# Kernel tuning notes

Measured on AMD Instinct MI355X. Metric: run time of the kernel, lower is better.

Reference implementation:

```python
import jax, jax.numpy as jnp
import numpy as np

IN_F, OUT_F, K, BATCH = 1024, 1024, 8, 4096


def setup_inputs() -> dict:
    key = jax.random.key(0)
    kx, ka, kb = jax.random.split(key, 3)
    x = jax.random.normal(kx, (BATCH, IN_F), dtype=jnp.float32)
    scale = 1.0 / (K * OUT_F)
    # a/b params: uniform in (-1,1)/(K*out_features), laid out [out, in, K]
    a = (2.0 * jax.random.uniform(ka, (OUT_F, IN_F, K)) - 1.0) * scale
    b = (2.0 * jax.random.uniform(kb, (OUT_F, IN_F, K)) - 1.0) * scale
    return {"x": x, "a": a.astype(jnp.float32), "b": b.astype(jnp.float32)}


def reference(x, a, b):
    # Fourier basis: k = 0..K-1 applied to every input feature
    K_ = a.shape[-1]
    ks = jnp.arange(K_, dtype=x.dtype)  # [K]
    phase = x[..., None] * ks  # [B, in, K]
    x_sin = jnp.sin(phase)
    x_cos = jnp.cos(phase)
    # y[b,o] = sum_{i,k} sin(k x_bi) a_oik + cos(k x_bi) b_oik
    y = jnp.einsum("bik,oik->bo", x_sin, a) + jnp.einsum("bik,oik->bo", x_cos, b)
    return y
```

## Files before the change

### kernel.cpp

```cpp
#include <hip/hip_runtime.h>

#define BATCH   4096
#define IN_F    1024
#define OUT_F   1024
#define KF      8
#define KD      14336

#define BM 256
#define BN 256
#define BK 64
#define KSPLIT 4
#define KCHUNK (KD/KSPLIT)
#define NT (KCHUNK/BK)
#define C_ELEMS ((size_t)BATCH * OUT_F)

#define QW 1040384.0f
#define DQ (1.0f/132128768.0f)

typedef int   i32x4 __attribute__((ext_vector_type(4)));
typedef float f32x4 __attribute__((ext_vector_type(4)));

__device__ __forceinline__ void gload_lds16(const void* g, void* l) {
  __builtin_amdgcn_global_load_lds((const __attribute__((address_space(1))) void*)g,
                                   (__attribute__((address_space(3))) void*)l,
                                   16, 0, 0);
}

__device__ __forceinline__ unsigned int pack4(int q0, int q1, int q2, int q3) {
  return (unsigned int)(q0 & 255) | ((unsigned int)(q1 & 255) << 8) |
         ((unsigned int)(q2 & 255) << 16) | ((unsigned int)(q3 & 255) << 24);
}

__global__ __launch_bounds__(256) void wconv_kernel(const float* __restrict__ a,
                                                    const float* __restrict__ b,
                                                    signed char* __restrict__ W,
                                                    float* __restrict__ bias) {
  const int o  = blockIdx.x;
  const int i0 = threadIdx.x * 4;
  const float4* ap = reinterpret_cast<const float4*>(a + (size_t)o * 8192 + i0 * 8);
  const float4* bp = reinterpret_cast<const float4*>(b + (size_t)o * 8192 + i0 * 8);
  union { float4 v[2]; float f[8]; } ua[4], ub[4];
#pragma unroll
  for (int ii = 0; ii < 4; ++ii) {
    ua[ii].v[0] = ap[2 * ii]; ua[ii].v[1] = ap[2 * ii + 1];
    ub[ii].v[0] = bp[2 * ii]; ub[ii].v[1] = bp[2 * ii + 1];
  }
  unsigned int* wp = reinterpret_cast<unsigned int*>(W + (size_t)o * KD + i0);
#pragma unroll
  for (int j = 0; j < 7; ++j) {
    int qa[4], qb[4];
#pragma unroll
    for (int ii = 0; ii < 4; ++ii) {
      qa[ii] = __float2int_rn(ua[ii].f[j + 1] * QW);
      qb[ii] = __float2int_rn(ub[ii].f[j + 1] * QW);
    }
    wp[j       * (IN_F / 4)] = pack4(qa[0], qa[1], qa[2], qa[3]);
    wp[(7 + j) * (IN_F / 4)] = pack4(qb[0], qb[1], qb[2], qb[3]);
  }
  float bsum = ub[0].f[0] + ub[1].f[0] + ub[2].f[0] + ub[3].f[0];
#pragma unroll
  for (int off = 32; off > 0; off >>= 1) bsum += __shfl_down(bsum, off);
  __shared__ float red[4];
  if ((threadIdx.x & 63) == 0) red[threadIdx.x >> 6] = bsum;
  __syncthreads();
  if (threadIdx.x == 0) bias[o] = red[0] + red[1] + red[2] + red[3];
}

__global__ __launch_bounds__(256) void feat_kernel(const float* __restrict__ x,
                                                   signed char* __restrict__ Xq) {
  int idx = blockIdx.x * 256 + threadIdx.x;
  int bb = idx >> 8;
  int i0 = (idx & 255) * 4;
  float4 xv = *reinterpret_cast<const float4*>(x + (size_t)bb * IN_F + i0);
  float sv[4][KF], cv[4][KF];
#pragma unroll
  for (int ii = 0; ii < 4; ++ii) {
    float xx = (ii == 0) ? xv.x : (ii == 1) ? xv.y : (ii == 2) ? xv.z : xv.w;
    sincosf(xx, &sv[ii][1], &cv[ii][1]);
#pragma unroll
    for (int k = 2; k < KF; ++k) {
      sv[ii][k] = sv[ii][k-1] * cv[ii][1] + cv[ii][k-1] * sv[ii][1];
      cv[ii][k] = cv[ii][k-1] * cv[ii][1] - sv[ii][k-1] * sv[ii][1];
    }
  }
  unsigned int* dst = reinterpret_cast<unsigned int*>(Xq + (size_t)bb * KD + i0);
#pragma unroll
  for (int j = 0; j < 7; ++j) {
    dst[j * (IN_F / 4)] = pack4(__float2int_rn(127.f * sv[0][j+1]), __float2int_rn(127.f * sv[1][j+1]),
                                __float2int_rn(127.f * sv[2][j+1]), __float2int_rn(127.f * sv[3][j+1]));
    dst[(7 + j) * (IN_F / 4)] = pack4(__float2int_rn(127.f * cv[0][j+1]), __float2int_rn(127.f * cv[1][j+1]),
                                      __float2int_rn(127.f * cv[2][j+1]), __float2int_rn(127.f * cv[3][j+1]));
  }
}

__global__ __launch_bounds__(512, 2) void gemm_kernel(const signed char* __restrict__ A,
                                                      const signed char* __restrict__ Bt,
                                                      int* __restrict__ Cout,
                                                      int use_slab) {
  __shared__ signed char sA[2][BM * BK];
  __shared__ signed char sB[2][BN * BK];

  const int tid  = threadIdx.x;
  const int wid  = tid >> 6;
  const int lane = tid & 63;
  const int wm = wid >> 2, wn = wid & 3;
  const int l15 = lane & 15;

  const int bid = blockIdx.x;
  const int s   = (bid & 7) * 32 + (bid >> 3);
  const int z   = s >> 6;
  const int mt  = s & 15;
  const int nt  = (s >> 4) & 3;
  const int m0  = mt * BM;
  const int n0  = nt * BN;
  const int fbase = z * KCHUNK;

  const int srow = wid * 16 + (lane >> 2);
  const int swz  = ((lane >> 2) & 3) ^ ((lane >> 4) & 3);
  const int gsrc = (lane & 3) ^ swz;
  const signed char* pA = A  + (size_t)(m0 + srow) * KD + fbase + gsrc * 16;
  const signed char* pB = Bt + (size_t)(n0 + srow) * KD + fbase + gsrc * 16;
  const int ldst = wid * 1024;

  const int rswz = (l15 & 3) ^ ((l15 >> 2) & 3);
  const int kgr  = (((lane >> 4) ^ rswz) & 3) * 16;
  const int arowb = (wm * 128 + l15) * BK;
  const int browb = (wn * 64 + l15) * BK;

  i32x4 acc[8][4] = {};

#define TILE(SAC, SBC, SAN, SBN_, KA, KB)                                       \
  {                                                                             \
    i32x4 af[8], bfr[4];                                                        \
    _Pragma("unroll") for (int f = 0; f < 8; ++f)                               \
      af[f] = *reinterpret_cast<const i32x4*>(                                  \
          (SAC) + arowb + f * (16 * BK) + kgr);                                 \
    _Pragma("unroll") for (int nf = 0; nf < 4; ++nf)                            \
      bfr[nf] = *reinterpret_cast<const i32x4*>(                                \
          (SBC) + browb + nf * (16 * BK) + kgr);                                \
    gload_lds16(pA + (KA), (SAN) + ldst);                                       \
    gload_lds16(pA + (size_t)128 * KD + (KA), (SAN) + 8192 + ldst);             \
    asm volatile("s_waitcnt lgkmcnt(0)" ::: "memory");                          \
    asm volatile("s_barrier" ::: "memory");                                     \
    gload_lds16(pB + (KB), (SBN_) + ldst);                                      \
    gload_lds16(pB + (size_t)128 * KD + (KB), (SBN_) + 8192 + ldst);            \
    __builtin_amdgcn_s_setprio(1);                                              \
    _Pragma("unroll") for (int f = 0; f < 8; ++f)                               \
      _Pragma("unroll") for (int nf = 0; nf < 4; ++nf)                          \
        acc[f][nf] = __builtin_amdgcn_mfma_i32_16x16x64_i8(                     \
            af[f], bfr[nf], acc[f][nf], 0, 0, 0);                               \
    __builtin_amdgcn_s_setprio(0);                                              \
    asm volatile("s_waitcnt vmcnt(2)" ::: "memory");                            \
    asm volatile("s_barrier" ::: "memory");                                     \
  }

  gload_lds16(pA,                        &sA[0][ldst]);
  gload_lds16(pA + (size_t)128 * KD,     &sA[0][8192 + ldst]);
  gload_lds16(pB,                        &sB[0][ldst]);
  gload_lds16(pB + (size_t)128 * KD,     &sB[0][8192 + ldst]);
  gload_lds16(pB + BK,                   &sB[1][ldst]);
  gload_lds16(pB + (size_t)128 * KD + BK, &sB[1][8192 + ldst]);
  asm volatile("s_waitcnt vmcnt(2)" ::: "memory");
  asm volatile("s_barrier" ::: "memory");

  for (int j = 0; j < NT / 2; ++j) {
    const int kA1 = (2 * j + 1) * BK;
    const int kB2 = (2 * j + 2 < NT) ? (2 * j + 2) * BK : 0;
    const int kB3 = (2 * j + 3 < NT) ? (2 * j + 3) * BK : 0;

    TILE(&sA[0][0], &sB[0][0], &sA[1][0], &sB[0][0], kA1, kB2)
    TILE(&sA[1][0], &sB[1][0], &sA[0][0], &sB[1][0], kB2, kB3)
  }
#undef TILE

  const int crow = m0 + wm * 128 + (lane >> 4) * 4;
  const int ccol = n0 + wn * 64 + l15;
  if (use_slab) {
    int* Cz = Cout + (size_t)z * C_ELEMS;
#pragma unroll
    for (int mf = 0; mf < 8; ++mf)
#pragma unroll
      for (int nf = 0; nf < 4; ++nf)
#pragma unroll
        for (int jj = 0; jj < 4; ++jj)
          Cz[(size_t)(crow + mf * 16 + jj) * OUT_F + ccol + nf * 16] = acc[mf][nf][jj];
  } else {
    float* Cf = reinterpret_cast<float*>(Cout);
#pragma unroll
    for (int mf = 0; mf < 8; ++mf)
#pragma unroll
      for (int nf = 0; nf < 4; ++nf)
#pragma unroll
        for (int jj = 0; jj < 4; ++jj)
          atomicAdd(&Cf[(size_t)(crow + mf * 16 + jj) * OUT_F + ccol + nf * 16],
                    (float)acc[mf][nf][jj] * DQ);
  }
}

__global__ __launch_bounds__(256) void reduce_kernel(const i32x4* __restrict__ s,
                                                     const float* __restrict__ bias,
                                                     f32x4* __restrict__ y) {
  size_t i = (size_t)blockIdx.x * 256 + threadIdx.x;
  const size_t NQ = C_ELEMS / 4;
  i32x4 v = s[i] + s[i + NQ] + s[i + 2 * NQ] + s[i + 3 * NQ];
  f32x4 bv = reinterpret_cast<const f32x4*>(bias)[i & 255];
  f32x4 r;
  r[0] = (float)v[0] * DQ + bv[0];
  r[1] = (float)v[1] * DQ + bv[1];
  r[2] = (float)v[2] * DQ + bv[2];
  r[3] = (float)v[3] * DQ + bv[3];
  y[i] = r;
}

__global__ __launch_bounds__(256) void binit_kernel(const float* __restrict__ bias,
                                                    f32x4* __restrict__ y) {
  size_t i = (size_t)blockIdx.x * 256 + threadIdx.x;
  y[i] = reinterpret_cast<const f32x4*>(bias)[i & 255];
}

__global__ __launch_bounds__(256) void naive_kernel(const float* __restrict__ x,
                                                    const float* __restrict__ a,
                                                    const float* __restrict__ b,
                                                    float* __restrict__ y) {
  int o  = blockIdx.x * 256 + threadIdx.x;
  int bb = blockIdx.y;
  __shared__ float xs[IN_F];
  for (int i = threadIdx.x; i < IN_F; i += 256) xs[i] = x[(size_t)bb * IN_F + i];
  __syncthreads();
  float acc = 0.f;
  for (int i = 0; i < IN_F; ++i) {
    float s1, c1; sincosf(xs[i], &s1, &c1);
    float sk = 0.f, ck = 1.f;
    const float* ap = a + (size_t)o * 8192 + i * KF;
    const float* bp = b + (size_t)o * 8192 + i * KF;
#pragma unroll
    for (int k = 0; k < KF; ++k) {
      acc += sk * ap[k] + ck * bp[k];
      float sn = sk * c1 + ck * s1;
      ck = ck * c1 - sk * s1;
      sk = sn;
    }
  }
  y[(size_t)bb * OUT_F + o] = acc;
}

extern "C" void kernel_launch(void* const* d_in, const int* in_sizes, int n_in,
                              void* d_out, int out_size, void* d_ws, size_t ws_size,
                              hipStream_t stream) {
  (void)in_sizes; (void)n_in; (void)out_size;
  const float* x = (const float*)d_in[0];
  const float* a = (const float*)d_in[1];
  const float* b = (const float*)d_in[2];
  float* y = (float*)d_out;

  const size_t XQ_BYTES   = (size_t)BATCH * KD;
  const size_t WQ_BYTES   = (size_t)OUT_F * KD;
  const size_t BIAS_BYTES = (size_t)OUT_F * sizeof(float);
  const size_t SLAB_BYTES = C_ELEMS * sizeof(int) * KSPLIT;

  if (ws_size >= XQ_BYTES + WQ_BYTES + BIAS_BYTES) {
    signed char* Xq = (signed char*)d_ws;
    signed char* Wq = (signed char*)d_ws + XQ_BYTES;
    float* bias     = (float*)((char*)d_ws + XQ_BYTES + WQ_BYTES);
    int* slabs      = (int*)((char*)d_ws + XQ_BYTES + WQ_BYTES + BIAS_BYTES);
    const bool slab = ws_size >= XQ_BYTES + WQ_BYTES + BIAS_BYTES + SLAB_BYTES;

    wconv_kernel<<<OUT_F, 256, 0, stream>>>(a, b, Wq, bias);
    feat_kernel<<<(BATCH * IN_F / 4) / 256, 256, 0, stream>>>(x, Xq);
    if (slab) {
      gemm_kernel<<<dim3((BATCH / BM) * (OUT_F / BN) * KSPLIT), 512, 0, stream>>>(Xq, Wq, slabs, 1);
      reduce_kernel<<<(int)(C_ELEMS / 4 / 256), 256, 0, stream>>>((const i32x4*)slabs, bias, (f32x4*)y);
    } else {
      binit_kernel<<<(int)(C_ELEMS / 4 / 256), 256, 0, stream>>>(bias, (f32x4*)y);
      gemm_kernel<<<dim3((BATCH / BM) * (OUT_F / BN) * KSPLIT), 512, 0, stream>>>(Xq, Wq, (int*)y, 0);
    }
  } else {
    naive_kernel<<<dim3(OUT_F / 256, BATCH), 256, 0, stream>>>(x, a, b, y);
  }
}
```

Baseline: 112.7 us.

## Triple-buffer B tiles and cut to one barrier per K-step in int8 GEMM

The GEMM main loop is restructured. A stays double-buffered in LDS while B gets a third LDS buffer, and the pointers rotate each iteration instead of using a two-tile unrolled macro. All global-to-LDS prefetches for the next A tile and the B tile two steps ahead are issued at the top of each iteration. This removes the mid-tile lgkmcnt wait and barrier, leaving one barrier per K-step. In exchange it raises LDS use to 80 KB per block (two blocks need 160 KB) and uses runtime pointer rotation, which may add address arithmetic.

```diff
diff --git a/kernel.cpp b/kernel.cpp
--- a/kernel.cpp
+++ b/kernel.cpp
@@ -98,7 +98,7 @@
                                                       int* __restrict__ Cout,
                                                       int use_slab) {
   __shared__ signed char sA[2][BM * BK];
-  __shared__ signed char sB[2][BN * BK];
+  __shared__ signed char sB[3][BN * BK];
 
   const int tid  = threadIdx.x;
   const int wid  = tid >> 6;
@@ -129,49 +129,49 @@
 
   i32x4 acc[8][4] = {};
 
-#define TILE(SAC, SBC, SAN, SBN_, KA, KB)                                       \
-  {                                                                             \
-    i32x4 af[8], bfr[4];                                                        \
-    _Pragma("unroll") for (int f = 0; f < 8; ++f)                               \
-      af[f] = *reinterpret_cast<const i32x4*>(                                  \
-          (SAC) + arowb + f * (16 * BK) + kgr);                                 \
-    _Pragma("unroll") for (int nf = 0; nf < 4; ++nf)                            \
-      bfr[nf] = *reinterpret_cast<const i32x4*>(                                \
-          (SBC) + browb + nf * (16 * BK) + kgr);                                \
-    gload_lds16(pA + (KA), (SAN) + ldst);                                       \
-    gload_lds16(pA + (size_t)128 * KD + (KA), (SAN) + 8192 + ldst);             \
-    asm volatile("s_waitcnt lgkmcnt(0)" ::: "memory");                          \
-    asm volatile("s_barrier" ::: "memory");                                     \
-    gload_lds16(pB + (KB), (SBN_) + ldst);                                      \
-    gload_lds16(pB + (size_t)128 * KD + (KB), (SBN_) + 8192 + ldst);            \
-    __builtin_amdgcn_s_setprio(1);                                              \
-    _Pragma("unroll") for (int f = 0; f < 8; ++f)                               \
-      _Pragma("unroll") for (int nf = 0; nf < 4; ++nf)                          \
-        acc[f][nf] = __builtin_amdgcn_mfma_i32_16x16x64_i8(                     \
-            af[f], bfr[nf], acc[f][nf], 0, 0, 0);                               \
-    __builtin_amdgcn_s_setprio(0);                                              \
-    asm volatile("s_waitcnt vmcnt(2)" ::: "memory");                            \
-    asm volatile("s_barrier" ::: "memory");                                     \
-  }
-
-  gload_lds16(pA,                        &sA[0][ldst]);
-  gload_lds16(pA + (size_t)128 * KD,     &sA[0][8192 + ldst]);
-  gload_lds16(pB,                        &sB[0][ldst]);
-  gload_lds16(pB + (size_t)128 * KD,     &sB[0][8192 + ldst]);
-  gload_lds16(pB + BK,                   &sB[1][ldst]);
+  gload_lds16(pA,                         &sA[0][ldst]);
+  gload_lds16(pA + (size_t)128 * KD,      &sA[0][8192 + ldst]);
+  gload_lds16(pB,                         &sB[0][ldst]);
+  gload_lds16(pB + (size_t)128 * KD,      &sB[0][8192 + ldst]);
+  gload_lds16(pB + BK,                    &sB[1][ldst]);
   gload_lds16(pB + (size_t)128 * KD + BK, &sB[1][8192 + ldst]);
   asm volatile("s_waitcnt vmcnt(2)" ::: "memory");
   asm volatile("s_barrier" ::: "memory");
 
-  for (int j = 0; j < NT / 2; ++j) {
-    const int kA1 = (2 * j + 1) * BK;
-    const int kB2 = (2 * j + 2 < NT) ? (2 * j + 2) * BK : 0;
-    const int kB3 = (2 * j + 3 < NT) ? (2 * j + 3) * BK : 0;
-
-    TILE(&sA[0][0], &sB[0][0], &sA[1][0], &sB[0][0], kA1, kB2)
-    TILE(&sA[1][0], &sB[1][0], &sA[0][0], &sB[1][0], kB2, kB3)
-  }
-#undef TILE
+  signed char* aR = &sA[0][0];  signed char* aS = &sA[1][0];
+  signed char* bR = &sB[0][0];  signed char* bN = &sB[1][0];  signed char* bS = &sB[2][0];
+
+  for (int t = 0; t < NT; ++t) {
+    const int kA = (t + 1 < NT) ? (t + 1) * BK : 0;
+    const int kB = (t + 2 < NT) ? (t + 2) * BK : 0;
+
+    gload_lds16(pA + kA,                      aS + ldst);
+    gload_lds16(pA + (size_t)128 * KD + kA,   aS + 8192 + ldst);
+    gload_lds16(pB + kB,                      bS + ldst);
+    gload_lds16(pB + (size_t)128 * KD + kB,   bS + 8192 + ldst);
+
+    i32x4 af[8], bfr[4];
+#pragma unroll
+    for (int f = 0; f < 8; ++f)
+      af[f] = *reinterpret_cast<const i32x4*>(aR + arowb + f * (16 * BK) + kgr);
+#pragma unroll
+    for (int nf = 0; nf < 4; ++nf)
+      bfr[nf] = *reinterpret_cast<const i32x4*>(bR + browb + nf * (16 * BK) + kgr);
+
+    __builtin_amdgcn_s_setprio(1);
+#pragma unroll
+    for (int f = 0; f < 8; ++f)
+#pragma unroll
+      for (int nf = 0; nf < 4; ++nf)
+        acc[f][nf] = __builtin_amdgcn_mfma_i32_16x16x64_i8(af[f], bfr[nf], acc[f][nf], 0, 0, 0);
+    __builtin_amdgcn_s_setprio(0);
+
+    asm volatile("s_waitcnt vmcnt(2)" ::: "memory");
+    asm volatile("s_barrier" ::: "memory");
+
+    signed char* tA = aR; aR = aS; aS = tA;
+    signed char* tB = bR; bR = bN; bN = bS; bS = tB;
+  }
 
   const int crow = m0 + wm * 128 + (lane >> 4) * 4;
   const int ccol = n0 + wn * 64 + l15;
```

After: 129.1 us. 1.15x slower.
